# Optimization experiments

Measured on AMD Instinct MI355X. Metric: run time of the kernel, lower is better.

The kernel has to match this reference:

```python
import jax, jax.numpy as jnp
import numpy as np

# Static DAG: input -> L hidden layers of K nodes (dense between layers) -> output.
B, WIDTH, K, L = 262144, 64, 4, 4


def _linear_init(key, shape, fan_in):
    # matches nn.Linear default: U(-1/sqrt(fan_in), 1/sqrt(fan_in))
    bound = 1.0 / np.sqrt(fan_in)
    return jax.random.uniform(key, shape, jnp.float32, -bound, bound)


def setup_inputs() -> dict:
    key = jax.random.key(0)
    ks = jax.random.split(key, 9)
    x = jax.random.normal(ks[0], (B, WIDTH), jnp.float32)
    # input node -> first hidden layer (K edges)
    W_in = _linear_init(ks[1], (K, WIDTH, WIDTH), WIDTH)
    b_in = _linear_init(ks[2], (K, WIDTH), WIDTH)
    # between hidden layers: (L-1) transitions, K*K edges each; [pred, node, out, in]
    W_mid = _linear_init(ks[3], (L - 1, K, K, WIDTH, WIDTH), WIDTH)
    b_mid = _linear_init(ks[4], (L - 1, K, K, WIDTH), WIDTH)
    # last hidden layer -> output node (K edges)
    W_out = _linear_init(ks[5], (K, WIDTH, WIDTH), WIDTH)
    b_out = _linear_init(ks[6], (K, WIDTH), WIDTH)
    return {"x": x, "W_in": W_in, "b_in": b_in, "W_mid": W_mid,
            "b_mid": b_mid, "W_out": W_out, "b_out": b_out}


def _l2_normalize(t):
    # torch.linalg.norm(t) with no dim: Frobenius norm over the WHOLE tensor
    return t / jnp.linalg.norm(t)


def reference(x, W_in, b_in, W_mid, b_mid, W_out, b_out):
    # input node -> layer 1: each node k gets a single edge Linear, then normalize
    h = jnp.einsum('bw,kvw->kbv', x, W_in) + b_in[:, None, :]  # [K,B,W]
    h = jax.vmap(_l2_normalize)(h)
    # hidden -> hidden transitions: node v sums over its K predecessor edges
    for l in range(L - 1):  # small fixed structural loop over layers
        pre = jnp.einsum('pbw,pkvw->kbv', h, W_mid[l]) + b_mid[l].sum(axis=0)[:, None, :]
        h = jax.vmap(_l2_normalize)(pre)
    # last layer -> output node: sum K edge outputs, normalize
    out = jnp.einsum('pbw,pvw->bv', h, W_out) + b_out.sum(axis=0)
    return _l2_normalize(out)
```

## Files before the change

kernel.cpp:

```cpp
#include <hip/hip_runtime.h>


#define BF 262144.0f

#define OFF_G   0
#define OFF_S   4096
#define OFF_P0  8192
#define OFF_P1  73728
#define OFF_C0  139264
#define OFF_C1  140288
#define OFF_MO  141312
#define OFF_CO  145408

typedef __attribute__((ext_vector_type(8))) short bf16x8;
typedef __attribute__((ext_vector_type(4))) float f32x4;

__device__ __forceinline__ unsigned short f2bf(float f) {
  unsigned u = __builtin_bit_cast(unsigned, f);
  u += 0x7FFF + ((u >> 16) & 1);
  return (unsigned short)(u >> 16);
}
__device__ __forceinline__ float bf2f(unsigned short h) {
  unsigned u = ((unsigned)h) << 16;
  return __builtin_bit_cast(float, u);
}

__device__ __forceinline__ bf16x8 cvt8(f32x4 a, f32x4 b, float s) {
  bf16x8 t;
#pragma unroll
  for (int j = 0; j < 4; j++) {
    t[j]     = (short)f2bf(a[j] * s);
    t[j + 4] = (short)f2bf(b[j] * s);
  }
  return t;
}

__global__ __launch_bounds__(256) void kG(const float* __restrict__ x,
                                          float* __restrict__ Gpart) {
  __shared__ __align__(16) unsigned short xts[4][4][16][8];
  __shared__ float sred[256][4];
  const int tid = threadIdx.x;
  const int lane = tid & 63, mt = tid >> 6;
  const int col = lane & 15, q = lane >> 4;
  const int row0 = tid >> 4;
  const int cf0  = (tid & 15) * 4;

  f32x4 acc[4];
#pragma unroll
  for (int nt = 0; nt < 4; nt++) acc[nt] = (f32x4){0.f, 0.f, 0.f, 0.f};
  float s0 = 0.f, s1 = 0.f, s2 = 0.f, s3 = 0.f;

  const float* bx = x + (long)blockIdx.x * 32768;
  f32x4 r0 = *(const f32x4*)(bx + tid * 4);
  f32x4 r1 = *(const f32x4*)(bx + 1024 + tid * 4);

  for (int c = 0; c < 16; c++) {
    __syncthreads();
    s0 += r0[0] + r1[0]; s1 += r0[1] + r1[1];
    s2 += r0[2] + r1[2]; s3 += r0[3] + r1[3];
#pragma unroll
    for (int j = 0; j < 4; j++) {
      const int cf = cf0 + j;
      xts[cf >> 4][row0 >> 3][cf & 15][row0 & 7]        = f2bf(r0[j]);
      xts[cf >> 4][2 + (row0 >> 3)][cf & 15][row0 & 7]  = f2bf(r1[j]);
    }
    f32x4 r0n = r0, r1n = r1;
    if (c < 15) {
      r0n = *(const f32x4*)(bx + (c + 1) * 2048 + tid * 4);
      r1n = *(const f32x4*)(bx + (c + 1) * 2048 + 1024 + tid * 4);
    }
    __syncthreads();
    const bf16x8 af = *(const bf16x8*)xts[mt][q][col];
#pragma unroll
    for (int nt = 0; nt < 4; nt++) {
      const bf16x8 bfr = *(const bf16x8*)xts[nt][q][col];
      acc[nt] = __builtin_amdgcn_mfma_f32_16x16x32_bf16(af, bfr, acc[nt], 0, 0, 0);
    }
    r0 = r0n; r1 = r1n;
  }

  float* myp = Gpart + (long)blockIdx.x * 4160;
#pragma unroll
  for (int nt = 0; nt < 4; nt++)
#pragma unroll
    for (int r = 0; r < 4; r++)
      myp[(mt * 16 + q * 4 + r) * 64 + nt * 16 + col] = acc[nt][r];

  sred[tid][0] = s0; sred[tid][1] = s1; sred[tid][2] = s2; sred[tid][3] = s3;
  __syncthreads();
  if (tid < 64) {
    float t = 0.f;
#pragma unroll
    for (int k2 = 0; k2 < 16; k2++) t += sred[(tid >> 2) + 16 * k2][tid & 3];
    myp[4096 + tid] = t;
  }
}

__global__ __launch_bounds__(256) void kGred(const float* __restrict__ Gpart,
                                             float* __restrict__ G,
                                             float* __restrict__ s) {
  __shared__ float red[4][64];
  const int tid = threadIdx.x;
  const int e = blockIdx.x * 64 + (tid & 63);
  const int quarter = tid >> 6;
  float acc = 0.f;
#pragma unroll 4
  for (int j = 0; j < 128; j++)
    acc += Gpart[(long)(quarter * 128 + j) * 4160 + e];
  red[quarter][tid & 63] = acc;
  __syncthreads();
  if (tid < 64) {
    const float t = red[0][tid] + red[1][tid] + red[2][tid] + red[3][tid];
    const int ee = blockIdx.x * 64 + tid;
    if (ee < 4096) G[ee] = t;
    else           s[ee - 4096] = t;
  }
}

__global__ __launch_bounds__(256) void kLayer(const float* __restrict__ Tsrc,
                                              const float* __restrict__ csrc,
                                              const float* __restrict__ Wm,
                                              const float* __restrict__ bm,
                                              const float* __restrict__ G,
                                              const float* __restrict__ s,
                                              float* __restrict__ Pout,
                                              float* __restrict__ cpout,
                                              const int KN, const int first) {
  __shared__ float Tf[64][68];
  __shared__ __align__(16) unsigned short Tth[64][68], Ttl[64][68];
  __shared__ __align__(16) unsigned short Wh[64][68], Wlo[64][68];
  __shared__ float red[256];
  __shared__ __align__(16) float cl[64], sl[64];
  const int tid = threadIdx.x;
  const int p = blockIdx.x / KN, kk = blockIdx.x % KN;
  const int lane = tid & 63, it = tid >> 6;
  const int col = lane & 15, quad = lane >> 4;

  float Greg[4][4];
#pragma unroll
  for (int ut = 0; ut < 4; ut++)
#pragma unroll
    for (int r = 0; r < 4; r++)
      Greg[ut][r] = G[(it * 16 + quad * 4 + r) * 64 + ut * 16 + col];

#pragma unroll
  for (int m = 0; m < 16; m++) {
    const int li = m * 256 + tid;
    const int r = li >> 6, cc = li & 63;
    float tv;
    if (first) tv = Tsrc[p * 4096 + li];
    else tv = Tsrc[p * 4096 + li] + Tsrc[(4 + p) * 4096 + li] +
              Tsrc[(8 + p) * 4096 + li] + Tsrc[(12 + p) * 4096 + li];
    Tf[r][cc] = tv;
    const float wv = Wm[(long)(p * KN + kk) * 4096 + li];
    const unsigned short wh = f2bf(wv);
    Wh[r][cc] = wh;
    Wlo[r][cc] = f2bf(wv - bf2f(wh));
  }
  if (tid < 64) {
    float cv;
    if (first) cv = csrc[p * 64 + tid];
    else cv = csrc[p * 64 + tid] + csrc[(4 + p) * 64 + tid] +
              csrc[(8 + p) * 64 + tid] + csrc[(12 + p) * 64 + tid];
    cl[tid] = cv;
    sl[tid] = s[tid];
  }
  __syncthreads();

  {
    const int tc = tid >> 2;
    const int rb = (tid & 3) * 16;
#pragma unroll
    for (int j = 0; j < 16; j++) {
      const float tv = Tf[rb + j][tc];
      const unsigned short h = f2bf(tv);
      Tth[tc][rb + j] = h;
      Ttl[tc][rb + j] = f2bf(tv - bf2f(h));
    }
  }
  __syncthreads();

  float qp = 0.f;
  {
    f32x4 dq[4];
#pragma unroll
    for (int ut = 0; ut < 4; ut++) dq[ut] = (f32x4){0.f, 0.f, 0.f, 0.f};
#pragma unroll
    for (int ks = 0; ks < 2; ks++) {
      const bf16x8 ah = *(const bf16x8*)&Tth[it * 16 + col][ks * 32 + quad * 8];
      const bf16x8 al = *(const bf16x8*)&Ttl[it * 16 + col][ks * 32 + quad * 8];
#pragma unroll
      for (int ut = 0; ut < 4; ut++) {
        const bf16x8 bh = *(const bf16x8*)&Tth[ut * 16 + col][ks * 32 + quad * 8];
        const bf16x8 bl = *(const bf16x8*)&Ttl[ut * 16 + col][ks * 32 + quad * 8];
        dq[ut] = __builtin_amdgcn_mfma_f32_16x16x32_bf16(ah, bh, dq[ut], 0, 0, 0);
        dq[ut] = __builtin_amdgcn_mfma_f32_16x16x32_bf16(ah, bl, dq[ut], 0, 0, 0);
        dq[ut] = __builtin_amdgcn_mfma_f32_16x16x32_bf16(al, bh, dq[ut], 0, 0, 0);
      }
    }
#pragma unroll
    for (int ut = 0; ut < 4; ut++)
#pragma unroll
      for (int r = 0; r < 4; r++)
        qp += dq[ut][r] * Greg[ut][r];
  }
  if (tid < 64) {
    float sd = 0.f;
#pragma unroll
    for (int u4 = 0; u4 < 16; u4++) {
      const f32x4 tv = *(const f32x4*)&Tf[tid][u4 * 4];
      const f32x4 sv = *(const f32x4*)&sl[u4 * 4];
      sd += sv[0] * tv[0] + sv[1] * tv[1] + sv[2] * tv[2] + sv[3] * tv[3];
    }
    qp += cl[tid] * (2.f * sd + BF * cl[tid]);
  }
  red[tid] = qp;
  __syncthreads();
  for (int st = 128; st > 0; st >>= 1) {
    if (tid < st) red[tid] += red[tid + st];
    __syncthreads();
  }
  const float inv = 1.0f / sqrtf(red[0]);

  {
    f32x4 dc[4];
#pragma unroll
    for (int nt = 0; nt < 4; nt++) dc[nt] = (f32x4){0.f, 0.f, 0.f, 0.f};
#pragma unroll
    for (int ks = 0; ks < 2; ks++) {
      const bf16x8 awh = *(const bf16x8*)&Wh[it * 16 + col][ks * 32 + quad * 8];
      const bf16x8 awl = *(const bf16x8*)&Wlo[it * 16 + col][ks * 32 + quad * 8];
#pragma unroll
      for (int nt = 0; nt < 4; nt++) {
        const bf16x8 bh = *(const bf16x8*)&Tth[nt * 16 + col][ks * 32 + quad * 8];
        const bf16x8 bl = *(const bf16x8*)&Ttl[nt * 16 + col][ks * 32 + quad * 8];
        dc[nt] = __builtin_amdgcn_mfma_f32_16x16x32_bf16(awh, bh, dc[nt], 0, 0, 0);
        dc[nt] = __builtin_amdgcn_mfma_f32_16x16x32_bf16(awh, bl, dc[nt], 0, 0, 0);
        dc[nt] = __builtin_amdgcn_mfma_f32_16x16x32_bf16(awl, bh, dc[nt], 0, 0, 0);
      }
    }
    float* po = Pout + (long)(p * KN + kk) * 4096;
#pragma unroll
    for (int nt = 0; nt < 4; nt++)
#pragma unroll
      for (int r = 0; r < 4; r++)
        po[(it * 16 + quad * 4 + r) * 64 + nt * 16 + col] = inv * dc[nt][r];
  }

  if (tid < 64) {
    const float* wg = Wm + (long)(p * KN + kk) * 4096 + tid * 64;
    float pc = 0.f;
#pragma unroll
    for (int u4 = 0; u4 < 16; u4++) {
      const f32x4 wv = *(const f32x4*)(wg + u4 * 4);
      pc += wv[0] * cl[u4 * 4] + wv[1] * cl[u4 * 4 + 1] +
            wv[2] * cl[u4 * 4 + 2] + wv[3] * cl[u4 * 4 + 3];
    }
    cpout[(p * KN + kk) * 64 + tid] = inv * pc + bm[(long)(p * KN + kk) * 64 + tid];
  }
}

__global__ __launch_bounds__(256) void kNorm(const float* __restrict__ Psrc,
                                             const float* __restrict__ csrc,
                                             const float* __restrict__ G,
                                             const float* __restrict__ s,
                                             float* __restrict__ MoS,
                                             float* __restrict__ coS) {
  __shared__ float Tf[64][68];
  __shared__ __align__(16) unsigned short Tth[64][68], Ttl[64][68];
  __shared__ float red[256];
  __shared__ __align__(16) float cl[64], sl[64];
  const int tid = threadIdx.x;
  const int lane = tid & 63, it = tid >> 6;
  const int col = lane & 15, quad = lane >> 4;

  float Greg[4][4];
#pragma unroll
  for (int ut = 0; ut < 4; ut++)
#pragma unroll
    for (int r = 0; r < 4; r++)
      Greg[ut][r] = G[(it * 16 + quad * 4 + r) * 64 + ut * 16 + col];

#pragma unroll
  for (int m = 0; m < 16; m++) {
    const int li = m * 256 + tid;
    Tf[li >> 6][li & 63] = Psrc[li] + Psrc[4096 + li] + Psrc[8192 + li] + Psrc[12288 + li];
  }
  if (tid < 64) {
    cl[tid] = csrc[tid] + csrc[64 + tid] + csrc[128 + tid] + csrc[192 + tid];
    sl[tid] = s[tid];
  }
  __syncthreads();

  {
    const int tc = tid >> 2;
    const int rb = (tid & 3) * 16;
#pragma unroll
    for (int j = 0; j < 16; j++) {
      const float tv = Tf[rb + j][tc];
      const unsigned short h = f2bf(tv);
      Tth[tc][rb + j] = h;
      Ttl[tc][rb + j] = f2bf(tv - bf2f(h));
    }
  }
  __syncthreads();

  float qp = 0.f;
  {
    f32x4 dq[4];
#pragma unroll
    for (int ut = 0; ut < 4; ut++) dq[ut] = (f32x4){0.f, 0.f, 0.f, 0.f};
#pragma unroll
    for (int ks = 0; ks < 2; ks++) {
      const bf16x8 ah = *(const bf16x8*)&Tth[it * 16 + col][ks * 32 + quad * 8];
      const bf16x8 al = *(const bf16x8*)&Ttl[it * 16 + col][ks * 32 + quad * 8];
#pragma unroll
      for (int ut = 0; ut < 4; ut++) {
        const bf16x8 bh = *(const bf16x8*)&Tth[ut * 16 + col][ks * 32 + quad * 8];
        const bf16x8 bl = *(const bf16x8*)&Ttl[ut * 16 + col][ks * 32 + quad * 8];
        dq[ut] = __builtin_amdgcn_mfma_f32_16x16x32_bf16(ah, bh, dq[ut], 0, 0, 0);
        dq[ut] = __builtin_amdgcn_mfma_f32_16x16x32_bf16(ah, bl, dq[ut], 0, 0, 0);
        dq[ut] = __builtin_amdgcn_mfma_f32_16x16x32_bf16(al, bh, dq[ut], 0, 0, 0);
      }
    }
#pragma unroll
    for (int ut = 0; ut < 4; ut++)
#pragma unroll
      for (int r = 0; r < 4; r++)
        qp += dq[ut][r] * Greg[ut][r];
  }
  if (tid < 64) {
    float sd = 0.f;
#pragma unroll
    for (int u4 = 0; u4 < 16; u4++) {
      const f32x4 tv = *(const f32x4*)&Tf[tid][u4 * 4];
      const f32x4 sv = *(const f32x4*)&sl[u4 * 4];
      sd += sv[0] * tv[0] + sv[1] * tv[1] + sv[2] * tv[2] + sv[3] * tv[3];
    }
    qp += cl[tid] * (2.f * sd + BF * cl[tid]);
  }
  red[tid] = qp;
  __syncthreads();
  for (int st = 128; st > 0; st >>= 1) {
    if (tid < st) red[tid] += red[tid + st];
    __syncthreads();
  }
  const float inv = 1.0f / sqrtf(red[0]);

#pragma unroll
  for (int m = 0; m < 16; m++) {
    const int li = m * 256 + tid;
    MoS[li] = inv * Tf[li >> 6][li & 63];
  }
  if (tid < 64) coS[tid] = inv * cl[tid];
}

__global__ __launch_bounds__(256) void kApply(const float* __restrict__ x,
                                              const float* __restrict__ MoS,
                                              const float* __restrict__ coS,
                                              float* __restrict__ out) {
  const int tid = threadIdx.x, lane = tid & 63, vt = tid >> 6;
  const int col = lane & 15, q = lane >> 4;

  bf16x8 bfr[2];
  const float* mr = MoS + (vt * 16 + col) * 64 + q * 8;
  bfr[0] = cvt8(*(const f32x4*)mr, *(const f32x4*)(mr + 4), 1.f);
  bfr[1] = cvt8(*(const f32x4*)(mr + 32), *(const f32x4*)(mr + 36), 1.f);
  const float cf = coS[vt * 16 + col];

  for (int t = 0; t < 16; t++) {
    const int b0 = (blockIdx.x * 16 + t) * 16;
    const float* xr = x + (long)(b0 + col) * 64 + q * 8;
    const bf16x8 a0 = cvt8(*(const f32x4*)xr, *(const f32x4*)(xr + 4), 1.f);
    const bf16x8 a1 = cvt8(*(const f32x4*)(xr + 32), *(const f32x4*)(xr + 36), 1.f);
    f32x4 acc = (f32x4){0.f, 0.f, 0.f, 0.f};
    acc = __builtin_amdgcn_mfma_f32_16x16x32_bf16(a0, bfr[0], acc, 0, 0, 0);
    acc = __builtin_amdgcn_mfma_f32_16x16x32_bf16(a1, bfr[1], acc, 0, 0, 0);
#pragma unroll
    for (int r = 0; r < 4; r++)
      out[(long)(b0 + q * 4 + r) * 64 + vt * 16 + col] = acc[r] + cf;
  }
}

extern "C" void kernel_launch(void* const* d_in, const int* in_sizes, int n_in,
                              void* d_out, int out_size, void* d_ws, size_t ws_size,
                              hipStream_t stream) {
  const float* x    = (const float*)d_in[0];
  const float* Win  = (const float*)d_in[1];
  const float* bin  = (const float*)d_in[2];
  const float* Wmid = (const float*)d_in[3];
  const float* bmid = (const float*)d_in[4];
  const float* Wout = (const float*)d_in[5];
  const float* bout = (const float*)d_in[6];
  float* out = (float*)d_out;
  float* ws  = (float*)d_ws;
  float* Gpart = out;

  kG   <<<512, 256, 0, stream>>>(x, Gpart);
  kGred<<<65, 256, 0, stream>>>(Gpart, ws + OFF_G, ws + OFF_S);
  kLayer<<<16, 256, 0, stream>>>(Win, bin, Wmid, bmid,
                                 ws + OFF_G, ws + OFF_S, ws + OFF_P0, ws + OFF_C0, 4, 1);
  kLayer<<<16, 256, 0, stream>>>(ws + OFF_P0, ws + OFF_C0, Wmid + 65536, bmid + 1024,
                                 ws + OFF_G, ws + OFF_S, ws + OFF_P1, ws + OFF_C1, 4, 0);
  kLayer<<<16, 256, 0, stream>>>(ws + OFF_P1, ws + OFF_C1, Wmid + 131072, bmid + 2048,
                                 ws + OFF_G, ws + OFF_S, ws + OFF_P0, ws + OFF_C0, 4, 0);
  kLayer<<<4, 256, 0, stream>>>(ws + OFF_P0, ws + OFF_C0, Wout, bout,
                                 ws + OFF_G, ws + OFF_S, ws + OFF_P1, ws + OFF_C1, 1, 0);
  kNorm<<<1, 256, 0, stream>>>(ws + OFF_P1, ws + OFF_C1, ws + OFF_G, ws + OFF_S,
                               ws + OFF_MO, ws + OFF_CO);
  kApply<<<1024, 256, 0, stream>>>(x, ws + OFF_MO, ws + OFF_CO, out);
}
```

Baseline: 233.9 us.

## Fuse four small layer-composition kernels into two chained kernels

Replaces the four sequential kLayer launches, which compose the per-layer 64x64 affine maps, with two kernels. Each new kernel recomputes the needed norm factors for all predecessors redundantly per block and then chains two layer compositions inside the block. This removes two launches and their global round trips on a latency-bound tiny chain. In exchange each block does redundant norm work, uses more dynamic shared memory, and the second kernel runs on only four blocks.

```diff
diff --git a/kernel.cpp b/kernel.cpp
--- a/kernel.cpp
+++ b/kernel.cpp
@@ -2,15 +2,16 @@
 
 
 #define BF 262144.0f
+#define SLOT 4608
 
 #define OFF_G   0
 #define OFF_S   4096
-#define OFF_P0  8192
-#define OFF_P1  73728
-#define OFF_C0  139264
-#define OFF_C1  140288
-#define OFF_MO  141312
-#define OFF_CO  145408
+#define OFF_P2  8192
+#define OFF_C2  73728
+#define OFF_P4  74752
+#define OFF_C4  91136
+#define OFF_MO  91392
+#define OFF_CO  95488
 
 typedef __attribute__((ext_vector_type(8))) short bf16x8;
 typedef __attribute__((ext_vector_type(4))) float f32x4;
@@ -33,6 +34,57 @@
     t[j + 4] = (short)f2bf(b[j] * s);
   }
   return t;
+}
+
+__device__ __forceinline__ void split8(f32x4 a, f32x4 b, float sc,
+                                       bf16x8& hi, bf16x8& lo) {
+#pragma unroll
+  for (int j = 0; j < 4; j++) {
+    float v = a[j] * sc;
+    unsigned short h = f2bf(v);
+    hi[j] = (short)h; lo[j] = (short)f2bf(v - bf2f(h));
+    v = b[j] * sc;
+    h = f2bf(v);
+    hi[j + 4] = (short)h; lo[j + 4] = (short)f2bf(v - bf2f(h));
+  }
+}
+
+__device__ __forceinline__ float qpart(const unsigned short* th,
+                                       const unsigned short* tl,
+                                       int it, int col, int quad,
+                                       const float Greg[4][4]) {
+  f32x4 dq[4];
+#pragma unroll
+  for (int ut = 0; ut < 4; ut++) dq[ut] = (f32x4){0.f, 0.f, 0.f, 0.f};
+#pragma unroll
+  for (int ks = 0; ks < 2; ks++) {
+    const bf16x8 ah = *(const bf16x8*)&th[(it * 16 + col) * 72 + ks * 32 + quad * 8];
+    const bf16x8 al = *(const bf16x8*)&tl[(it * 16 + col) * 72 + ks * 32 + quad * 8];
+#pragma unroll
+    for (int ut = 0; ut < 4; ut++) {
+      const bf16x8 bh = *(const bf16x8*)&th[(ut * 16 + col) * 72 + ks * 32 + quad * 8];
+      const bf16x8 bl = *(const bf16x8*)&tl[(ut * 16 + col) * 72 + ks * 32 + quad * 8];
+      dq[ut] = __builtin_amdgcn_mfma_f32_16x16x32_bf16(ah, bh, dq[ut], 0, 0, 0);
+      dq[ut] = __builtin_amdgcn_mfma_f32_16x16x32_bf16(ah, bl, dq[ut], 0, 0, 0);
+      dq[ut] = __builtin_amdgcn_mfma_f32_16x16x32_bf16(al, bh, dq[ut], 0, 0, 0);
+    }
+  }
+  float qp = 0.f;
+#pragma unroll
+  for (int ut = 0; ut < 4; ut++)
+#pragma unroll
+    for (int r = 0; r < 4; r++) qp += dq[ut][r] * Greg[ut][r];
+  return qp;
+}
+
+__device__ __forceinline__ void blkred(float qp, float* red4, float* qvv,
+                                       int idx, int tid, int lane, int it) {
+#pragma unroll
+  for (int off = 32; off; off >>= 1) qp += __shfl_down(qp, off, 64);
+  if (lane == 0) red4[it] = qp;
+  __syncthreads();
+  if (tid == 0) qvv[idx] = 1.0f / sqrtf(red4[0] + red4[1] + red4[2] + red4[3]);
+  __syncthreads();
 }
 
 __global__ __launch_bounds__(256) void kG(const float* __restrict__ x,
@@ -117,22 +169,23 @@
   }
 }
 
-__global__ __launch_bounds__(256) void kLayer(const float* __restrict__ Tsrc,
-                                              const float* __restrict__ csrc,
-                                              const float* __restrict__ Wm,
-                                              const float* __restrict__ bm,
-                                              const float* __restrict__ G,
-                                              const float* __restrict__ s,
-                                              float* __restrict__ Pout,
-                                              float* __restrict__ cpout,
-                                              const int KN, const int first) {
-  __shared__ float Tf[64][68];
-  __shared__ __align__(16) unsigned short Tth[64][68], Ttl[64][68];
-  __shared__ __align__(16) unsigned short Wh[64][68], Wlo[64][68];
-  __shared__ float red[256];
-  __shared__ __align__(16) float cl[64], sl[64];
+__global__ __launch_bounds__(256) void kChainA(
+    const float* __restrict__ Win, const float* __restrict__ bin,
+    const float* __restrict__ Wm0, const float* __restrict__ bm0,
+    const float* __restrict__ Wm1, const float* __restrict__ bm1,
+    const float* __restrict__ G, const float* __restrict__ s,
+    float* __restrict__ Pout, float* __restrict__ cpout) {
+  extern __shared__ __align__(16) char smem[];
+  unsigned short* Tth = (unsigned short*)smem;
+  unsigned short* Ttl = Tth + 4 * SLOT;
+  float* cAv  = (float*)(Ttl + 4 * SLOT);
+  float* cBv  = cAv + 256;
+  float* slv  = cBv + 64;
+  float* red4 = slv + 64;
+  float* qvv  = red4 + 4;
+
   const int tid = threadIdx.x;
-  const int p = blockIdx.x / KN, kk = blockIdx.x % KN;
+  const int p2 = blockIdx.x >> 2, k2 = blockIdx.x & 3;
   const int lane = tid & 63, it = tid >> 6;
   const int col = lane & 15, quad = lane >> 4;
 
@@ -142,121 +195,347 @@
 #pragma unroll
     for (int r = 0; r < 4; r++)
       Greg[ut][r] = G[(it * 16 + quad * 4 + r) * 64 + ut * 16 + col];
-
-#pragma unroll
-  for (int m = 0; m < 16; m++) {
-    const int li = m * 256 + tid;
-    const int r = li >> 6, cc = li & 63;
-    float tv;
-    if (first) tv = Tsrc[p * 4096 + li];
-    else tv = Tsrc[p * 4096 + li] + Tsrc[(4 + p) * 4096 + li] +
-              Tsrc[(8 + p) * 4096 + li] + Tsrc[(12 + p) * 4096 + li];
-    Tf[r][cc] = tv;
-    const float wv = Wm[(long)(p * KN + kk) * 4096 + li];
-    const unsigned short wh = f2bf(wv);
-    Wh[r][cc] = wh;
-    Wlo[r][cc] = f2bf(wv - bf2f(wh));
-  }
-  if (tid < 64) {
-    float cv;
-    if (first) cv = csrc[p * 64 + tid];
-    else cv = csrc[p * 64 + tid] + csrc[(4 + p) * 64 + tid] +
-              csrc[(8 + p) * 64 + tid] + csrc[(12 + p) * 64 + tid];
-    cl[tid] = cv;
-    sl[tid] = s[tid];
-  }
-  __syncthreads();
-
-  {
-    const int tc = tid >> 2;
-    const int rb = (tid & 3) * 16;
-#pragma unroll
-    for (int j = 0; j < 16; j++) {
-      const float tv = Tf[rb + j][tc];
-      const unsigned short h = f2bf(tv);
-      Tth[tc][rb + j] = h;
-      Ttl[tc][rb + j] = f2bf(tv - bf2f(h));
-    }
-  }
-  __syncthreads();
-
-  float qp = 0.f;
-  {
-    f32x4 dq[4];
-#pragma unroll
-    for (int ut = 0; ut < 4; ut++) dq[ut] = (f32x4){0.f, 0.f, 0.f, 0.f};
-#pragma unroll
-    for (int ks = 0; ks < 2; ks++) {
-      const bf16x8 ah = *(const bf16x8*)&Tth[it * 16 + col][ks * 32 + quad * 8];
-      const bf16x8 al = *(const bf16x8*)&Ttl[it * 16 + col][ks * 32 + quad * 8];
-#pragma unroll
-      for (int ut = 0; ut < 4; ut++) {
-        const bf16x8 bh = *(const bf16x8*)&Tth[ut * 16 + col][ks * 32 + quad * 8];
-        const bf16x8 bl = *(const bf16x8*)&Ttl[ut * 16 + col][ks * 32 + quad * 8];
-        dq[ut] = __builtin_amdgcn_mfma_f32_16x16x32_bf16(ah, bh, dq[ut], 0, 0, 0);
-        dq[ut] = __builtin_amdgcn_mfma_f32_16x16x32_bf16(ah, bl, dq[ut], 0, 0, 0);
-        dq[ut] = __builtin_amdgcn_mfma_f32_16x16x32_bf16(al, bh, dq[ut], 0, 0, 0);
+  if (tid < 64) slv[tid] = s[tid];
+  if (tid < 256) cAv[tid] = bin[tid];
+
+  {
+    const int tc = tid >> 2, rb = (tid & 3) * 16;
+#pragma unroll
+    for (int p = 0; p < 4; p++)
+#pragma unroll
+      for (int j = 0; j < 16; j++) {
+        const float tv = Win[p * 4096 + (rb + j) * 64 + tc];
+        const unsigned short h = f2bf(tv);
+        Tth[p * SLOT + tc * 72 + rb + j] = h;
+        Ttl[p * SLOT + tc * 72 + rb + j] = f2bf(tv - bf2f(h));
       }
-    }
-#pragma unroll
-    for (int ut = 0; ut < 4; ut++)
+  }
+  __syncthreads();
+
+#pragma unroll
+  for (int p = 0; p < 4; p++) {
+    float qp = qpart(Tth + p * SLOT, Ttl + p * SLOT, it, col, quad, Greg);
+    if (tid < 64) {
+      float sd = 0.f;
+      for (int w = 0; w < 64; w++)
+        sd += slv[w] * (bf2f(Tth[p * SLOT + w * 72 + tid]) +
+                        bf2f(Ttl[p * SLOT + w * 72 + tid]));
+      const float c = cAv[p * 64 + tid];
+      qp += c * (2.f * sd + BF * c);
+    }
+    blkred(qp, red4, qvv, p, tid, lane, it);
+  }
+
+  f32x4 dc[4];
+#pragma unroll
+  for (int nt = 0; nt < 4; nt++) dc[nt] = (f32x4){0.f, 0.f, 0.f, 0.f};
+  float c2acc = 0.f;
+
+  const int arow = it * 16 + col;
+  f32x4 wr[4];
+  {
+    const float* wbase = Wm0 + (long)((0 * 4 + p2) * 64 + arow) * 64;
+    wr[0] = *(const f32x4*)(wbase + quad * 8);
+    wr[1] = *(const f32x4*)(wbase + quad * 8 + 4);
+    wr[2] = *(const f32x4*)(wbase + 32 + quad * 8);
+    wr[3] = *(const f32x4*)(wbase + 36 + quad * 8);
+  }
+#pragma unroll
+  for (int p = 0; p < 4; p++) {
+    const float inv = qvv[p];
+    bf16x8 awh0, awl0, awh1, awl1;
+    split8(wr[0], wr[1], inv, awh0, awl0);
+    split8(wr[2], wr[3], inv, awh1, awl1);
+    if (p < 3) {
+      const float* wbase = Wm0 + (long)(((p + 1) * 4 + p2) * 64 + arow) * 64;
+      wr[0] = *(const f32x4*)(wbase + quad * 8);
+      wr[1] = *(const f32x4*)(wbase + quad * 8 + 4);
+      wr[2] = *(const f32x4*)(wbase + 32 + quad * 8);
+      wr[3] = *(const f32x4*)(wbase + 36 + quad * 8);
+    }
+#pragma unroll
+    for (int nt = 0; nt < 4; nt++) {
+      const bf16x8 bh0 = *(const bf16x8*)&Tth[p * SLOT + (nt * 16 + col) * 72 + quad * 8];
+      const bf16x8 bl0 = *(const bf16x8*)&Ttl[p * SLOT + (nt * 16 + col) * 72 + quad * 8];
+      dc[nt] = __builtin_amdgcn_mfma_f32_16x16x32_bf16(awh0, bh0, dc[nt], 0, 0, 0);
+      dc[nt] = __builtin_amdgcn_mfma_f32_16x16x32_bf16(awh0, bl0, dc[nt], 0, 0, 0);
+      dc[nt] = __builtin_amdgcn_mfma_f32_16x16x32_bf16(awl0, bh0, dc[nt], 0, 0, 0);
+      const bf16x8 bh1 = *(const bf16x8*)&Tth[p * SLOT + (nt * 16 + col) * 72 + 32 + quad * 8];
+      const bf16x8 bl1 = *(const bf16x8*)&Ttl[p * SLOT + (nt * 16 + col) * 72 + 32 + quad * 8];
+      dc[nt] = __builtin_amdgcn_mfma_f32_16x16x32_bf16(awh1, bh1, dc[nt], 0, 0, 0);
+      dc[nt] = __builtin_amdgcn_mfma_f32_16x16x32_bf16(awh1, bl1, dc[nt], 0, 0, 0);
+      dc[nt] = __builtin_amdgcn_mfma_f32_16x16x32_bf16(awl1, bh1, dc[nt], 0, 0, 0);
+    }
+    if (tid < 64) {
+      const float* wrow = Wm0 + (long)((p * 4 + p2) * 64 + tid) * 64;
+      float pc = 0.f;
+#pragma unroll
+      for (int u4 = 0; u4 < 16; u4++) {
+        const f32x4 wv = *(const f32x4*)(wrow + u4 * 4);
+        pc += wv[0] * cAv[p * 64 + u4 * 4]     + wv[1] * cAv[p * 64 + u4 * 4 + 1] +
+              wv[2] * cAv[p * 64 + u4 * 4 + 2] + wv[3] * cAv[p * 64 + u4 * 4 + 3];
+      }
+      c2acc += inv * pc + bm0[(p * 4 + p2) * 64 + tid];
+    }
+  }
+  __syncthreads();
+
+#pragma unroll
+  for (int nt = 0; nt < 4; nt++)
+#pragma unroll
+    for (int r = 0; r < 4; r++) {
+      const float val = dc[nt][r];
+      const unsigned short h = f2bf(val);
+      const int w_ = nt * 16 + col, v_ = it * 16 + quad * 4 + r;
+      Tth[w_ * 72 + v_] = h;
+      Ttl[w_ * 72 + v_] = f2bf(val - bf2f(h));
+    }
+  if (tid < 64) cBv[tid] = c2acc;
+  __syncthreads();
+
+  {
+    float qp = qpart(Tth, Ttl, it, col, quad, Greg);
+    if (tid < 64) {
+      float sd = 0.f;
+      for (int w = 0; w < 64; w++)
+        sd += slv[w] * (bf2f(Tth[w * 72 + tid]) + bf2f(Ttl[w * 72 + tid]));
+      const float c = cBv[tid];
+      qp += c * (2.f * sd + BF * c);
+    }
+    blkred(qp, red4, qvv, 4, tid, lane, it);
+  }
+  const float inv2 = qvv[4];
+
+  {
+    f32x4 dcO[4];
+#pragma unroll
+    for (int nt = 0; nt < 4; nt++) dcO[nt] = (f32x4){0.f, 0.f, 0.f, 0.f};
+    const float* wbase = Wm1 + (long)((p2 * 4 + k2) * 64 + arow) * 64;
+    const f32x4 w0 = *(const f32x4*)(wbase + quad * 8);
+    const f32x4 w1 = *(const f32x4*)(wbase + quad * 8 + 4);
+    const f32x4 w2 = *(const f32x4*)(wbase + 32 + quad * 8);
+    const f32x4 w3 = *(const f32x4*)(wbase + 36 + quad * 8);
+    bf16x8 awh0, awl0, awh1, awl1;
+    split8(w0, w1, inv2, awh0, awl0);
+    split8(w2, w3, inv2, awh1, awl1);
+#pragma unroll
+    for (int nt = 0; nt < 4; nt++) {
+      const bf16x8 bh0 = *(const bf16x8*)&Tth[(nt * 16 + col) * 72 + quad * 8];
+      const bf16x8 bl0 = *(const bf16x8*)&Ttl[(nt * 16 + col) * 72 + quad * 8];
+      dcO[nt] = __builtin_amdgcn_mfma_f32_16x16x32_bf16(awh0, bh0, dcO[nt], 0, 0, 0);
+      dcO[nt] = __builtin_amdgcn_mfma_f32_16x16x32_bf16(awh0, bl0, dcO[nt], 0, 0, 0);
+      dcO[nt] = __builtin_amdgcn_mfma_f32_16x16x32_bf16(awl0, bh0, dcO[nt], 0, 0, 0);
+      const bf16x8 bh1 = *(const bf16x8*)&Tth[(nt * 16 + col) * 72 + 32 + quad * 8];
+      const bf16x8 bl1 = *(const bf16x8*)&Ttl[(nt * 16 + col) * 72 + 32 + quad * 8];
+      dcO[nt] = __builtin_amdgcn_mfma_f32_16x16x32_bf16(awh1, bh1, dcO[nt], 0, 0, 0);
+      dcO[nt] = __builtin_amdgcn_mfma_f32_16x16x32_bf16(awh1, bl1, dcO[nt], 0, 0, 0);
+      dcO[nt] = __builtin_amdgcn_mfma_f32_16x16x32_bf16(awl1, bh1, dcO[nt], 0, 0, 0);
+    }
+    float* po = Pout + (long)(p2 * 4 + k2) * 4096;
+#pragma unroll
+    for (int nt = 0; nt < 4; nt++)
 #pragma unroll
       for (int r = 0; r < 4; r++)
-        qp += dq[ut][r] * Greg[ut][r];
-  }
-  if (tid < 64) {
-    float sd = 0.f;
-#pragma unroll
-    for (int u4 = 0; u4 < 16; u4++) {
-      const f32x4 tv = *(const f32x4*)&Tf[tid][u4 * 4];
-      const f32x4 sv = *(const f32x4*)&sl[u4 * 4];
-      sd += sv[0] * tv[0] + sv[1] * tv[1] + sv[2] * tv[2] + sv[3] * tv[3];
-    }
-    qp += cl[tid] * (2.f * sd + BF * cl[tid]);
-  }
-  red[tid] = qp;
-  __syncthreads();
-  for (int st = 128; st > 0; st >>= 1) {
-    if (tid < st) red[tid] += red[tid + st];
-    __syncthreads();
-  }
-  const float inv = 1.0f / sqrtf(red[0]);
-
-  {
-    f32x4 dc[4];
-#pragma unroll
-    for (int nt = 0; nt < 4; nt++) dc[nt] = (f32x4){0.f, 0.f, 0.f, 0.f};
-#pragma unroll
-    for (int ks = 0; ks < 2; ks++) {
-      const bf16x8 awh = *(const bf16x8*)&Wh[it * 16 + col][ks * 32 + quad * 8];
-      const bf16x8 awl = *(const bf16x8*)&Wlo[it * 16 + col][ks * 32 + quad * 8];
-#pragma unroll
-      for (int nt = 0; nt < 4; nt++) {
-        const bf16x8 bh = *(const bf16x8*)&Tth[nt * 16 + col][ks * 32 + quad * 8];
-        const bf16x8 bl = *(const bf16x8*)&Ttl[nt * 16 + col][ks * 32 + quad * 8];
-        dc[nt] = __builtin_amdgcn_mfma_f32_16x16x32_bf16(awh, bh, dc[nt], 0, 0, 0);
-        dc[nt] = __builtin_amdgcn_mfma_f32_16x16x32_bf16(awh, bl, dc[nt], 0, 0, 0);
-        dc[nt] = __builtin_amdgcn_mfma_f32_16x16x32_bf16(awl, bh, dc[nt], 0, 0, 0);
+        po[(it * 16 + quad * 4 + r) * 64 + nt * 16 + col] = dcO[nt][r];
+    if (tid < 64) {
+      const float* wrow = Wm1 + (long)((p2 * 4 + k2) * 64 + tid) * 64;
+      float pc = 0.f;
+#pragma unroll
+      for (int u4 = 0; u4 < 16; u4++) {
+        const f32x4 wv = *(const f32x4*)(wrow + u4 * 4);
+        pc += wv[0] * cBv[u4 * 4]     + wv[1] * cBv[u4 * 4 + 1] +
+              wv[2] * cBv[u4 * 4 + 2] + wv[3] * cBv[u4 * 4 + 3];
       }
-    }
-    float* po = Pout + (long)(p * KN + kk) * 4096;
+      cpout[(p2 * 4 + k2) * 64 + tid] = inv2 * pc + bm1[(p2 * 4 + k2) * 64 + tid];
+    }
+  }
+}
+
+__global__ __launch_bounds__(256) void kChainB(
+    const float* __restrict__ Pin, const float* __restrict__ cpin,
+    const float* __restrict__ Wm2, const float* __restrict__ bm2,
+    const float* __restrict__ Wout, const float* __restrict__ bout,
+    const float* __restrict__ G, const float* __restrict__ s,
+    float* __restrict__ Pout, float* __restrict__ cpout) {
+  extern __shared__ __align__(16) char smem[];
+  unsigned short* Tth = (unsigned short*)smem;
+  unsigned short* Ttl = Tth + 4 * SLOT;
+  float* cAv  = (float*)(Ttl + 4 * SLOT);
+  float* cBv  = cAv + 256;
+  float* slv  = cBv + 64;
+  float* red4 = slv + 64;
+  float* qvv  = red4 + 4;
+
+  const int tid = threadIdx.x;
+  const int kp = blockIdx.x;
+  const int lane = tid & 63, it = tid >> 6;
+  const int col = lane & 15, quad = lane >> 4;
+
+  float Greg[4][4];
+#pragma unroll
+  for (int ut = 0; ut < 4; ut++)
+#pragma unroll
+    for (int r = 0; r < 4; r++)
+      Greg[ut][r] = G[(it * 16 + quad * 4 + r) * 64 + ut * 16 + col];
+  if (tid < 64) slv[tid] = s[tid];
+  if (tid < 256) {
+    const int k = tid >> 6, v = tid & 63;
+    cAv[tid] = cpin[(0 * 4 + k) * 64 + v] + cpin[(1 * 4 + k) * 64 + v] +
+               cpin[(2 * 4 + k) * 64 + v] + cpin[(3 * 4 + k) * 64 + v];
+  }
+
+  {
+    const int tc = tid >> 2, rb = (tid & 3) * 16;
+#pragma unroll
+    for (int k = 0; k < 4; k++)
+#pragma unroll
+      for (int j = 0; j < 16; j++) {
+        const int off = (rb + j) * 64 + tc;
+        const float tv = Pin[(0 * 4 + k) * 4096 + off] + Pin[(1 * 4 + k) * 4096 + off] +
+                         Pin[(2 * 4 + k) * 4096 + off] + Pin[(3 * 4 + k) * 4096 + off];
+        const unsigned short h = f2bf(tv);
+        Tth[k * SLOT + tc * 72 + rb + j] = h;
+        Ttl[k * SLOT + tc * 72 + rb + j] = f2bf(tv - bf2f(h));
+      }
+  }
+  __syncthreads();
+
+#pragma unroll
+  for (int k = 0; k < 4; k++) {
+    float qp = qpart(Tth + k * SLOT, Ttl + k * SLOT, it, col, quad, Greg);
+    if (tid < 64) {
+      float sd = 0.f;
+      for (int w = 0; w < 64; w++)
+        sd += slv[w] * (bf2f(Tth[k * SLOT + w * 72 + tid]) +
+                        bf2f(Ttl[k * SLOT + w * 72 + tid]));
+      const float c = cAv[k * 64 + tid];
+      qp += c * (2.f * sd + BF * c);
+    }
+    blkred(qp, red4, qvv, k, tid, lane, it);
+  }
+
+  f32x4 dc[4];
+#pragma unroll
+  for (int nt = 0; nt < 4; nt++) dc[nt] = (f32x4){0.f, 0.f, 0.f, 0.f};
+  float c4acc = 0.f;
+
+  const int arow = it * 16 + col;
+  f32x4 wr[4];
+  {
+    const float* wbase = Wm2 + (long)((0 * 4 + kp) * 64 + arow) * 64;
+    wr[0] = *(const f32x4*)(wbase + quad * 8);
+    wr[1] = *(const f32x4*)(wbase + quad * 8 + 4);
+    wr[2] = *(const f32x4*)(wbase + 32 + quad * 8);
+    wr[3] = *(const f32x4*)(wbase + 36 + quad * 8);
+  }
+#pragma unroll
+  for (int k = 0; k < 4; k++) {
+    const float inv = qvv[k];
+    bf16x8 awh0, awl0, awh1, awl1;
+    split8(wr[0], wr[1], inv, awh0, awl0);
+    split8(wr[2], wr[3], inv, awh1, awl1);
+    if (k < 3) {
+      const float* wbase = Wm2 + (long)(((k + 1) * 4 + kp) * 64 + arow) * 64;
+      wr[0] = *(const f32x4*)(wbase + quad * 8);
+      wr[1] = *(const f32x4*)(wbase + quad * 8 + 4);
+      wr[2] = *(const f32x4*)(wbase + 32 + quad * 8);
+      wr[3] = *(const f32x4*)(wbase + 36 + quad * 8);
+    }
+#pragma unroll
+    for (int nt = 0; nt < 4; nt++) {
+      const bf16x8 bh0 = *(const bf16x8*)&Tth[k * SLOT + (nt * 16 + col) * 72 + quad * 8];
+      const bf16x8 bl0 = *(const bf16x8*)&Ttl[k * SLOT + (nt * 16 + col) * 72 + quad * 8];
+      dc[nt] = __builtin_amdgcn_mfma_f32_16x16x32_bf16(awh0, bh0, dc[nt], 0, 0, 0);
+      dc[nt] = __builtin_amdgcn_mfma_f32_16x16x32_bf16(awh0, bl0, dc[nt], 0, 0, 0);
+      dc[nt] = __builtin_amdgcn_mfma_f32_16x16x32_bf16(awl0, bh0, dc[nt], 0, 0, 0);
+      const bf16x8 bh1 = *(const bf16x8*)&Tth[k * SLOT + (nt * 16 + col) * 72 + 32 + quad * 8];
+      const bf16x8 bl1 = *(const bf16x8*)&Ttl[k * SLOT + (nt * 16 + col) * 72 + 32 + quad * 8];
+      dc[nt] = __builtin_amdgcn_mfma_f32_16x16x32_bf16(awh1, bh1, dc[nt], 0, 0, 0);
+      dc[nt] = __builtin_amdgcn_mfma_f32_16x16x32_bf16(awh1, bl1, dc[nt], 0, 0, 0);
+      dc[nt] = __builtin_amdgcn_mfma_f32_16x16x32_bf16(awl1, bh1, dc[nt], 0, 0, 0);
+    }
+    if (tid < 64) {
+      const float* wrow = Wm2 + (long)((k * 4 + kp) * 64 + tid) * 64;
+      float pc = 0.f;
+#pragma unroll
+      for (int u4 = 0; u4 < 16; u4++) {
+        const f32x4 wv = *(const f32x4*)(wrow + u4 * 4);
+        pc += wv[0] * cAv[k * 64 + u4 * 4]     + wv[1] * cAv[k * 64 + u4 * 4 + 1] +
+              wv[2] * cAv[k * 64 + u4 * 4 + 2] + wv[3] * cAv[k * 64 + u4 * 4 + 3];
+      }
+      c4acc += inv * pc + bm2[(k * 4 + kp) * 64 + tid];
+    }
+  }
+  __syncthreads();
+
+#pragma unroll
+  for (int nt = 0; nt < 4; nt++)
+#pragma unroll
+    for (int r = 0; r < 4; r++) {
+      const float val = dc[nt][r];
+      const unsigned short h = f2bf(val);
+      const int w_ = nt * 16 + col, v_ = it * 16 + quad * 4 + r;
+      Tth[w_ * 72 + v_] = h;
+      Ttl[w_ * 72 + v_] = f2bf(val - bf2f(h));
+    }
+  if (tid < 64) cBv[tid] = c4acc;
+  __syncthreads();
+
+  {
+    float qp = qpart(Tth, Ttl, it, col, quad, Greg);
+    if (tid < 64) {
+      float sd = 0.f;
+      for (int w = 0; w < 64; w++)
+        sd += slv[w] * (bf2f(Tth[w * 72 + tid]) + bf2f(Ttl[w * 72 + tid]));
+      const float c = cBv[tid];
+      qp += c * (2.f * sd + BF * c);
+    }
+    blkred(qp, red4, qvv, 4, tid, lane, it);
+  }
+  const float inv4 = qvv[4];
+
+  {
+    f32x4 dcO[4];
+#pragma unroll
+    for (int nt = 0; nt < 4; nt++) dcO[nt] = (f32x4){0.f, 0.f, 0.f, 0.f};
+    const float* wbase = Wout + (long)(kp * 64 + arow) * 64;
+    const f32x4 w0 = *(const f32x4*)(wbase + quad * 8);
+    const f32x4 w1 = *(const f32x4*)(wbase + quad * 8 + 4);
+    const f32x4 w2 = *(const f32x4*)(wbase + 32 + quad * 8);
+    const f32x4 w3 = *(const f32x4*)(wbase + 36 + quad * 8);
+    bf16x8 awh0, awl0, awh1, awl1;
+    split8(w0, w1, inv4, awh0, awl0);
+    split8(w2, w3, inv4, awh1, awl1);
+#pragma unroll
+    for (int nt = 0; nt < 4; nt++) {
+      const bf16x8 bh0 = *(const bf16x8*)&Tth[(nt * 16 + col) * 72 + quad * 8];
+      const bf16x8 bl0 = *(const bf16x8*)&Ttl[(nt * 16 + col) * 72 + quad * 8];
+      dcO[nt] = __builtin_amdgcn_mfma_f32_16x16x32_bf16(awh0, bh0, dcO[nt], 0, 0, 0);
+      dcO[nt] = __builtin_amdgcn_mfma_f32_16x16x32_bf16(awh0, bl0, dcO[nt], 0, 0, 0);
+      dcO[nt] = __builtin_amdgcn_mfma_f32_16x16x32_bf16(awl0, bh0, dcO[nt], 0, 0, 0);
+      const bf16x8 bh1 = *(const bf16x8*)&Tth[(nt * 16 + col) * 72 + 32 + quad * 8];
+      const bf16x8 bl1 = *(const bf16x8*)&Ttl[(nt * 16 + col) * 72 + 32 + quad * 8];
+      dcO[nt] = __builtin_amdgcn_mfma_f32_16x16x32_bf16(awh1, bh1, dcO[nt], 0, 0, 0);
+      dcO[nt] = __builtin_amdgcn_mfma_f32_16x16x32_bf16(awh1, bl1, dcO[nt], 0, 0, 0);
+      dcO[nt] = __builtin_amdgcn_mfma_f32_16x16x32_bf16(awl1, bh1, dcO[nt], 0, 0, 0);
+    }
+    float* po = Pout + (long)kp * 4096;
 #pragma unroll
     for (int nt = 0; nt < 4; nt++)
 #pragma unroll
       for (int r = 0; r < 4; r++)
-        po[(it * 16 + quad * 4 + r) * 64 + nt * 16 + col] = inv * dc[nt][r];
-  }
-
-  if (tid < 64) {
-    const float* wg = Wm + (long)(p * KN + kk) * 4096 + tid * 64;
-    float pc = 0.f;
-#pragma unroll
-    for (int u4 = 0; u4 < 16; u4++) {
-      const f32x4 wv = *(const f32x4*)(wg + u4 * 4);
-      pc += wv[0] * cl[u4 * 4] + wv[1] * cl[u4 * 4 + 1] +
-            wv[2] * cl[u4 * 4 + 2] + wv[3] * cl[u4 * 4 + 3];
-    }
-    cpout[(p * KN + kk) * 64 + tid] = inv * pc + bm[(long)(p * KN + kk) * 64 + tid];
+        po[(it * 16 + quad * 4 + r) * 64 + nt * 16 + col] = dcO[nt][r];
+    if (tid < 64) {
+      const float* wrow = Wout + (long)(kp * 64 + tid) * 64;
+      float pc = 0.f;
+#pragma unroll
+      for (int u4 = 0; u4 < 16; u4++) {
+        const f32x4 wv = *(const f32x4*)(wrow + u4 * 4);
+        pc += wv[0] * cBv[u4 * 4]     + wv[1] * cBv[u4 * 4 + 1] +
+              wv[2] * cBv[u4 * 4 + 2] + wv[3] * cBv[u4 * 4 + 3];
+      }
+      cpout[kp * 64 + tid] = inv4 * pc + bout[kp * 64 + tid];
+    }
   }
 }
 
@@ -396,17 +675,20 @@
   float* ws  = (float*)d_ws;
   float* Gpart = out;
 
+  const size_t SMEM = (size_t)(8 * SLOT) * 2 + 396 * 4 + 64;
+  hipFuncSetAttribute((const void*)kChainA,
+                      hipFuncAttributeMaxDynamicSharedMemorySize, (int)SMEM);
+  hipFuncSetAttribute((const void*)kChainB,
+                      hipFuncAttributeMaxDynamicSharedMemorySize, (int)SMEM);
+
   kG   <<<512, 256, 0, stream>>>(x, Gpart);
   kGred<<<65, 256, 0, stream>>>(Gpart, ws + OFF_G, ws + OFF_S);
-  kLayer<<<16, 256, 0, stream>>>(Win, bin, Wmid, bmid,
-                                 ws + OFF_G, ws + OFF_S, ws + OFF_P0, ws + OFF_C0, 4, 1);
-  kLayer<<<16, 256, 0, stream>>>(ws + OFF_P0, ws + OFF_C0, Wmid + 65536, bmid + 1024,
-                                 ws + OFF_G, ws + OFF_S, ws + OFF_P1, ws + OFF_C1, 4, 0);
-  kLayer<<<16, 256, 0, stream>>>(ws + OFF_P1, ws + OFF_C1, Wmid + 131072, bmid + 2048,
-                                 ws + OFF_G, ws + OFF_S, ws + OFF_P0, ws + OFF_C0, 4, 0);
-  kLayer<<<4, 256, 0, stream>>>(ws + OFF_P0, ws + OFF_C0, Wout, bout,
-                                 ws + OFF_G, ws + OFF_S, ws + OFF_P1, ws + OFF_C1, 1, 0);
-  kNorm<<<1, 256, 0, stream>>>(ws + OFF_P1, ws + OFF_C1, ws + OFF_G, ws + OFF_S,
+  kChainA<<<16, 256, SMEM, stream>>>(Win, bin, Wmid, bmid, Wmid + 65536, bmid + 1024,
+                                     ws + OFF_G, ws + OFF_S, ws + OFF_P2, ws + OFF_C2);
+  kChainB<<<4, 256, SMEM, stream>>>(ws + OFF_P2, ws + OFF_C2,
+                                    Wmid + 131072, bmid + 2048, Wout, bout,
+                                    ws + OFF_G, ws + OFF_S, ws + OFF_P4, ws + OFF_C4);
+  kNorm<<<1, 256, 0, stream>>>(ws + OFF_P4, ws + OFF_C4, ws + OFF_G, ws + OFF_S,
                                ws + OFF_MO, ws + OFF_CO);
   kApply<<<1024, 256, 0, stream>>>(x, ws + OFF_MO, ws + OFF_CO, out);
 }
```

After: 230.8 us. No clear change (-1.3%).
